# Kernel optimization log

Measured on AMD Instinct MI355X. Metric: run time of the kernel, lower is better.

## Reference

```python
import jax, jax.numpy as jnp
import numpy as np

N_HEAD = 16
N_EMBD = 1024


def setup_inputs() -> dict:
    key = jax.random.key(0)
    k1, k2, k3 = jax.random.split(key, 3)
    B, T = 2, 2048
    x = jax.random.normal(k1, (B, T, N_EMBD), dtype=jnp.float32)
    w_attn = jax.random.normal(k2, (N_EMBD, 3 * N_EMBD), dtype=jnp.float32) * 0.02
    b_attn = jnp.zeros((3 * N_EMBD,), dtype=jnp.float32)
    w_proj = jax.random.normal(k3, (N_EMBD, N_EMBD), dtype=jnp.float32) * 0.02
    b_proj = jnp.zeros((N_EMBD,), dtype=jnp.float32)
    return {"x": x, "w_attn": w_attn, "b_attn": b_attn, "w_proj": w_proj, "b_proj": b_proj}


def _split_heads(t):
    # [B, T, E] -> [B, H, T, hd]
    B, T, E = t.shape
    return t.reshape(B, T, N_HEAD, E // N_HEAD).transpose(0, 2, 1, 3)


def reference(x, w_attn, b_attn, w_proj, b_proj):
    B, T, E = x.shape
    hd = E // N_HEAD
    c = x @ w_attn + b_attn                       # [B, T, 3E]
    q, k, v = jnp.split(c, 3, axis=2)
    q, k, v = _split_heads(q), _split_heads(k), _split_heads(v)  # [B,H,T,hd]
    present = jnp.stack((k, v), axis=1)           # [B, 2, H, T, hd]
    # scores, scaled by rsqrt(head_dim)
    w = jnp.einsum("bhqd,bhkd->bhqk", q, k) * jax.lax.rsqrt(jnp.float32(hd))
    # causal mask: w * mask + -1e9 * (1 - mask)  (faithful to the source)
    mask = jnp.tril(jnp.ones((T, T), dtype=w.dtype))[None, None]
    w = w * mask + (-1e9) * (1.0 - mask)
    w = jax.nn.softmax(w, axis=-1)
    a = jnp.einsum("bhqk,bhkd->bhqd", w, v)       # [B,H,T,hd]
    a = a.transpose(0, 2, 1, 3).reshape(B, T, E)  # merge heads
    a = a @ w_proj + b_proj
    return a, present
```

## Files before the change

kernel.cpp:

```cpp
#include <hip/hip_runtime.h>

typedef unsigned short u16b;
typedef __attribute__((ext_vector_type(4))) float f32x4;
typedef __attribute__((ext_vector_type(8))) short bf16x8;

#define GLD_LDS(g, l) __builtin_amdgcn_global_load_lds( \
    (__attribute__((address_space(1))) void*)(g), \
    (__attribute__((address_space(3))) void*)(l), 16, 0, 0)

__device__ __forceinline__ u16b f2bf(float f) {
    unsigned u = __builtin_bit_cast(unsigned, f);
    u += 0x7fffu + ((u >> 16) & 1u);
    return (u16b)(u >> 16);
}
__device__ __forceinline__ unsigned trunc_bf(float f) {
    return __builtin_bit_cast(unsigned, f) >> 16;
}

__global__ void prep(const float* __restrict__ x, u16b* __restrict__ xb,
                     const float* __restrict__ w_attn, u16b* __restrict__ wab,
                     const float* __restrict__ w_proj, u16b* __restrict__ wpb) {
    __shared__ float tile[32][33];
    const int blk = blockIdx.x;
    if (blk < 4096) {
        int i = blk * 256 + threadIdx.x;
        float4 v = ((const float4*)x)[i];
        uint2 o;
        o.x = (unsigned)f2bf(v.x) | ((unsigned)f2bf(v.y) << 16);
        o.y = (unsigned)f2bf(v.z) | ((unsigned)f2bf(v.w) << 16);
        ((uint2*)xb)[i] = o;
        return;
    }
    const float* in;
    u16b* out;
    int idx, N;
    if (blk < 7168) { idx = blk - 4096; N = 3072; in = w_attn; out = wab; }
    else            { idx = blk - 7168; N = 1024; in = w_proj; out = wpb; }
    const int K = 1024;
    int kt = (idx & 31) * 32, nt = (idx >> 5) * 32;
    int c = threadIdx.x & 31, r8 = threadIdx.x >> 5;
    for (int i = 0; i < 4; i++) {
        int r = r8 + i * 8;
        tile[r][c] = in[(size_t)(kt + r) * N + nt + c];
    }
    __syncthreads();
    for (int i = 0; i < 4; i++) {
        int r = r8 + i * 8;
        out[(size_t)(nt + r) * K + kt + c] = f2bf(tile[c][r]);
    }
}

__global__ void trans_v(const u16b* __restrict__ in, u16b* __restrict__ out) {
    __shared__ u16b tile[64][66];
    const int bh = blockIdx.y;
    const int t0 = blockIdx.x * 64;
    const u16b* ip = in + (size_t)bh * 2048 * 64 + (size_t)t0 * 64;
    u16b* op = out + (size_t)bh * 64 * 2048 + t0;
    const int c = threadIdx.x & 7, r = threadIdx.x >> 3;
    #pragma unroll
    for (int it = 0; it < 2; it++) {
        int row = it * 32 + r;
        uint4 v = *(const uint4*)(ip + row * 64 + c * 8);
        const u16b* pv = (const u16b*)&v;
        #pragma unroll
        for (int e = 0; e < 8; e++) tile[c * 8 + e][row] = pv[e];
    }
    __syncthreads();
    const int d = threadIdx.x >> 2, c2 = threadIdx.x & 3;
    uint4 o[2];
    u16b* po = (u16b*)o;
    #pragma unroll
    for (int k = 0; k < 16; k++) po[k] = tile[d][c2 * 16 + k];
    *(uint4*)(op + d * 2048 + c2 * 16) = o[0];
    *(uint4*)(op + d * 2048 + c2 * 16 + 8) = o[1];
}

template<int EPI, int MI, int NI>
__global__ __launch_bounds__(256, 2) void gemm_bt(
    const u16b* __restrict__ A, const u16b* __restrict__ Bt,
    int M, int N, int K,
    const float* __restrict__ bias,
    float* __restrict__ out_f,
    u16b* __restrict__ q_ws, u16b* __restrict__ k_ws, u16b* __restrict__ v_ws)
{
    __shared__ u16b sA[(MI * 32) * 64];
    __shared__ u16b sB[(NI * 32) * 64];
    const int tid = threadIdx.x;
    const int l = tid & 63, w = tid >> 6;
    const int lr = l & 15, lg = l >> 4;
    const int m0 = blockIdx.y * (MI * 32), n0 = blockIdx.x * (NI * 32);
    const int wm = (w >> 1) * (MI * 16), wn = (w & 1) * (NI * 16);
    f32x4 acc[MI][NI] = {};

    for (int kt = 0; kt < K; kt += 64) {
        #pragma unroll
        for (int i = 0; i < MI; i++) {
            int chunk = i * 256 + tid;
            int row = chunk >> 3;
            int cb = (chunk & 7) ^ (row & 7);
            GLD_LDS(A + (size_t)(m0 + row) * K + kt + cb * 8, &sA[(i * 256 + w * 64) * 8]);
        }
        #pragma unroll
        for (int i = 0; i < NI; i++) {
            int chunk = i * 256 + tid;
            int row = chunk >> 3;
            int cb = (chunk & 7) ^ (row & 7);
            GLD_LDS(Bt + (size_t)(n0 + row) * K + kt + cb * 8, &sB[(i * 256 + w * 64) * 8]);
        }
        __syncthreads();
        #pragma unroll
        for (int ks = 0; ks < 2; ks++) {
            bf16x8 af[MI], bf[NI];
            #pragma unroll
            for (int i = 0; i < MI; i++) {
                int arow = wm + i * 16 + lr;
                af[i] = *(const bf16x8*)((const char*)sA + arow * 128 + ((ks * 64 + lg * 16) ^ ((arow & 7) << 4)));
            }
            #pragma unroll
            for (int i = 0; i < NI; i++) {
                int brow = wn + i * 16 + lr;
                bf[i] = *(const bf16x8*)((const char*)sB + brow * 128 + ((ks * 64 + lg * 16) ^ ((brow & 7) << 4)));
            }
            #pragma unroll
            for (int mi = 0; mi < MI; mi++)
                #pragma unroll
                for (int ni = 0; ni < NI; ni++)
                    acc[mi][ni] = __builtin_amdgcn_mfma_f32_16x16x32_bf16(af[mi], bf[ni], acc[mi][ni], 0, 0, 0);
        }
        __syncthreads();
    }

    if (EPI == 1) {
        #pragma unroll
        for (int ni = 0; ni < NI; ni++) {
            int col = n0 + wn + ni * 16 + lr;
            float bv = bias[col];
            #pragma unroll
            for (int mi = 0; mi < MI; mi++)
                #pragma unroll
                for (int jj = 0; jj < 4; jj++) {
                    int rowm = m0 + wm + mi * 16 + lg * 4 + jj;
                    out_f[(size_t)rowm * N + col] = acc[mi][ni][jj] + bv;
                }
        }
    } else {
        const int qkv = n0 >> 10;
        #pragma unroll
        for (int ni = 0; ni < NI; ni++) {
            int n = n0 + wn + ni * 16 + lr;
            float bv = bias[n];
            int h = (n >> 6) & 15, d = n & 63;
            #pragma unroll
            for (int mi = 0; mi < MI; mi++)
                #pragma unroll
                for (int jj = 0; jj < 4; jj++) {
                    int m = m0 + wm + mi * 16 + lg * 4 + jj;
                    int b = m >> 11, t = m & 2047;
                    float c = acc[mi][ni][jj] + bv;
                    size_t bhtd = ((size_t)(b * 16 + h) * 2048 + t) * 64 + d;
                    if (qkv == 0) {
                        q_ws[bhtd] = f2bf(c * 0.18033688011f);
                    } else if (qkv == 1) {
                        out_f[((size_t)((b * 2 + 0) * 16 + h) * 2048 + t) * 64 + d] = c;
                        k_ws[bhtd] = f2bf(c);
                    } else {
                        out_f[((size_t)((b * 2 + 1) * 16 + h) * 2048 + t) * 64 + d] = c;
                        v_ws[bhtd] = f2bf(c);
                    }
                }
        }
    }
}

__global__ __launch_bounds__(256, 4) void attn_fwd(
    const u16b* __restrict__ q_ws, const u16b* __restrict__ k_ws,
    const u16b* __restrict__ v_t, u16b* __restrict__ a_ws)
{
    __shared__ u16b sK[2][64 * 64];
    __shared__ u16b sV[2][64 * 64];
    __shared__ u16b sP[4][16 * 64];
    const int tid = threadIdx.x;
    const int l = tid & 63, w = tid >> 6;
    const int lr = l & 15, lg = l >> 4;
    const int g = blockIdx.x >> 5, bh = blockIdx.x & 31;
    const int a = g & 7, bq = g >> 3;
    const int qt = (bq == 0) ? a : (bq == 1) ? 15 - a : (bq == 2) ? 16 + a : 31 - a;
    const int b = bh >> 4, h = bh & 15;
    const size_t kbase = (size_t)bh * 2048 * 64;
    const size_t vbase = (size_t)bh * 64 * 2048;

    const int chunk0 = tid, chunk1 = 256 + tid;
    const int row0 = chunk0 >> 3, cb0 = (chunk0 & 7) ^ (row0 & 7);
    const int row1 = chunk1 >> 3, cb1 = (chunk1 & 7) ^ (row1 & 7);
    const u16b* kp0 = k_ws + kbase + (size_t)row0 * 64 + cb0 * 8;
    const u16b* kp1 = k_ws + kbase + (size_t)row1 * 64 + cb1 * 8;
    const u16b* vp0 = v_t + vbase + (size_t)row0 * 2048 + cb0 * 8;
    const u16b* vp1 = v_t + vbase + (size_t)row1 * 2048 + cb1 * 8;

    bf16x8 qf[2];
    {
        const u16b* qp = q_ws + kbase + (size_t)(qt * 64 + w * 16 + lr) * 64 + lg * 8;
        qf[0] = *(const bf16x8*)qp;
        qf[1] = *(const bf16x8*)(qp + 32);
    }
    const bf16x8 ones = {0x3F80, 0x3F80, 0x3F80, 0x3F80, 0x3F80, 0x3F80, 0x3F80, 0x3F80};
    f32x4 Oacc[4] = {};
    f32x4 Lacc = {};

    GLD_LDS(kp0, &sK[0][chunk0 * 8]);
    GLD_LDS(kp1, &sK[0][chunk1 * 8]);
    GLD_LDS(vp0, &sV[0][chunk0 * 8]);
    GLD_LDS(vp1, &sV[0][chunk1 * 8]);
    __syncthreads();
    int cur = 0;

    #pragma unroll 1
    for (int j = 0; j <= qt; j++) {
        if (j < qt) {
            int nxt = cur ^ 1;
            size_t ko = (size_t)(j + 1) * 64 * 64;
            size_t vo = (size_t)(j + 1) * 64;
            GLD_LDS(kp0 + ko, &sK[nxt][chunk0 * 8]);
            GLD_LDS(kp1 + ko, &sK[nxt][chunk1 * 8]);
            GLD_LDS(vp0 + vo, &sV[nxt][chunk0 * 8]);
            GLD_LDS(vp1 + vo, &sV[nxt][chunk1 * 8]);
        }
        const u16b* cK = &sK[cur][0];
        const u16b* cV = &sV[cur][0];

        f32x4 S[4];
        __builtin_amdgcn_s_setprio(1);
        #pragma unroll
        for (int c = 0; c < 4; c++) {
            f32x4 s = {};
            #pragma unroll
            for (int ks = 0; ks < 2; ks++) {
                int krow = c * 16 + lr;
                bf16x8 kf = *(const bf16x8*)((const char*)cK + krow * 128 + ((ks * 64 + lg * 16) ^ ((krow & 7) << 4)));
                s = __builtin_amdgcn_mfma_f32_16x16x32_bf16(kf, qf[ks], s, 0, 0, 0);
            }
            S[c] = s;
        }
        __builtin_amdgcn_s_setprio(0);
        if (j == qt) {
            const int ql = w * 16 + lr;
            #pragma unroll
            for (int c = 0; c < 4; c++)
                #pragma unroll
                for (int jj = 0; jj < 4; jj++)
                    if (c * 16 + lg * 4 + jj > ql) S[c][jj] = -1e9f;
        }
        u16b* myP = &sP[w][0];
        #pragma unroll
        for (int c = 0; c < 4; c++) {
            #pragma unroll
            for (int jj = 0; jj < 4; jj++)
                S[c][jj] = __builtin_amdgcn_exp2f(S[c][jj]);
            uint2 pk;
            pk.x = trunc_bf(S[c][0]) | (trunc_bf(S[c][1]) << 16);
            pk.y = trunc_bf(S[c][2]) | (trunc_bf(S[c][3]) << 16);
            *(uint2*)((char*)myP + lr * 128 + ((c * 32 + lg * 8) ^ ((lr & 7) << 4))) = pk;
        }
        __builtin_amdgcn_s_setprio(1);
        #pragma unroll
        for (int ks = 0; ks < 2; ks++) {
            bf16x8 pa = *(const bf16x8*)((const char*)myP + lr * 128 + ((ks * 64 + lg * 16) ^ ((lr & 7) << 4)));
            #pragma unroll
            for (int dc = 0; dc < 4; dc++) {
                int vrow = dc * 16 + lr;
                bf16x8 vb = *(const bf16x8*)((const char*)cV + vrow * 128 + ((ks * 64 + lg * 16) ^ ((vrow & 7) << 4)));
                Oacc[dc] = __builtin_amdgcn_mfma_f32_16x16x32_bf16(pa, vb, Oacc[dc], 0, 0, 0);
            }
            Lacc = __builtin_amdgcn_mfma_f32_16x16x32_bf16(pa, ones, Lacc, 0, 0, 0);
        }
        __builtin_amdgcn_s_setprio(0);
        __syncthreads();
        cur ^= 1;
    }
    #pragma unroll
    for (int jj = 0; jj < 4; jj++) {
        float inv = 1.f / Lacc[jj];
        int q = qt * 64 + w * 16 + lg * 4 + jj;
        #pragma unroll
        for (int dc = 0; dc < 4; dc++) {
            int d = dc * 16 + lr;
            a_ws[(size_t)(b * 2048 + q) * 1024 + h * 64 + d] = f2bf(Oacc[dc][jj] * inv);
        }
    }
}

extern "C" void kernel_launch(void* const* d_in, const int* in_sizes, int n_in,
                              void* d_out, int out_size, void* d_ws, size_t ws_size,
                              hipStream_t stream) {
    const float* x      = (const float*)d_in[0];
    const float* w_attn = (const float*)d_in[1];
    const float* b_attn = (const float*)d_in[2];
    const float* w_proj = (const float*)d_in[3];
    const float* b_proj = (const float*)d_in[4];
    float* out = (float*)d_out;
    float* present = out + 4194304;

    char* ws = (char*)d_ws;
    u16b* xb   = (u16b*)(ws);
    u16b* wab  = (u16b*)(ws + 8388608);
    u16b* wpb  = (u16b*)(ws + 14680064);
    u16b* q_ws = (u16b*)(ws + 16777216);
    u16b* k_ws = (u16b*)(ws + 25165824);
    u16b* v_ws = (u16b*)(ws + 33554432);
    u16b* a_ws = (u16b*)(ws + 41943040);
    u16b* v_t  = xb;

    prep<<<8192, 256, 0, stream>>>(x, xb, w_attn, wab, w_proj, wpb);
    gemm_bt<0, 2, 4><<<dim3(24, 64), 256, 0, stream>>>(xb, wab, 4096, 3072, 1024, b_attn,
                                                       present, q_ws, k_ws, v_ws);
    trans_v<<<dim3(32, 32), 256, 0, stream>>>(v_ws, v_t);
    attn_fwd<<<1024, 256, 0, stream>>>(q_ws, k_ws, v_t, a_ws);
    gemm_bt<1, 2, 2><<<dim3(16, 64), 256, 0, stream>>>(a_ws, wpb, 4096, 1024, 1024, b_proj,
                                                       out, nullptr, nullptr, nullptr);
}
```

Baseline: 115.5 us.

## Widen attention query tile to 128 rows with 8 waves sharing K/V loads

The attention kernel now uses 512-thread blocks with 8 waves covering 128 query rows, so each K/V tile loaded into LDS is reused by twice as many queries and the number of blocks is halved. Causal masking is applied over the last two KV tiles, and load balancing pairs query tiles g and 23-g. The QKV GEMM also switches to a larger M tile configuration with half the grid rows. The cost is fewer, heavier blocks, which may reduce occupancy and makes the causal diagonal waste more work per block.

```diff
diff --git a/kernel.cpp b/kernel.cpp
--- a/kernel.cpp
+++ b/kernel.cpp
@@ -172,58 +172,48 @@
     }
 }
 
-__global__ __launch_bounds__(256, 4) void attn_fwd(
+__global__ __launch_bounds__(512, 2) void attn_fwd(
     const u16b* __restrict__ q_ws, const u16b* __restrict__ k_ws,
     const u16b* __restrict__ v_t, u16b* __restrict__ a_ws)
 {
     __shared__ u16b sK[2][64 * 64];
     __shared__ u16b sV[2][64 * 64];
-    __shared__ u16b sP[4][16 * 64];
+    __shared__ u16b sP[8][16 * 64];
     const int tid = threadIdx.x;
     const int l = tid & 63, w = tid >> 6;
     const int lr = l & 15, lg = l >> 4;
     const int g = blockIdx.x >> 5, bh = blockIdx.x & 31;
-    const int a = g & 7, bq = g >> 3;
-    const int qt = (bq == 0) ? a : (bq == 1) ? 15 - a : (bq == 2) ? 16 + a : 31 - a;
+    const int qt = (g < 8) ? g : 23 - g;
     const int b = bh >> 4, h = bh & 15;
     const size_t kbase = (size_t)bh * 2048 * 64;
     const size_t vbase = (size_t)bh * 64 * 2048;
 
-    const int chunk0 = tid, chunk1 = 256 + tid;
-    const int row0 = chunk0 >> 3, cb0 = (chunk0 & 7) ^ (row0 & 7);
-    const int row1 = chunk1 >> 3, cb1 = (chunk1 & 7) ^ (row1 & 7);
+    const int row0 = tid >> 3, cb0 = (tid & 7) ^ (row0 & 7);
     const u16b* kp0 = k_ws + kbase + (size_t)row0 * 64 + cb0 * 8;
-    const u16b* kp1 = k_ws + kbase + (size_t)row1 * 64 + cb1 * 8;
     const u16b* vp0 = v_t + vbase + (size_t)row0 * 2048 + cb0 * 8;
-    const u16b* vp1 = v_t + vbase + (size_t)row1 * 2048 + cb1 * 8;
 
     bf16x8 qf[2];
     {
-        const u16b* qp = q_ws + kbase + (size_t)(qt * 64 + w * 16 + lr) * 64 + lg * 8;
+        const u16b* qp = q_ws + kbase + (size_t)(qt * 128 + w * 16 + lr) * 64 + lg * 8;
         qf[0] = *(const bf16x8*)qp;
         qf[1] = *(const bf16x8*)(qp + 32);
     }
     const bf16x8 ones = {0x3F80, 0x3F80, 0x3F80, 0x3F80, 0x3F80, 0x3F80, 0x3F80, 0x3F80};
     f32x4 Oacc[4] = {};
     f32x4 Lacc = {};
-
-    GLD_LDS(kp0, &sK[0][chunk0 * 8]);
-    GLD_LDS(kp1, &sK[0][chunk1 * 8]);
-    GLD_LDS(vp0, &sV[0][chunk0 * 8]);
-    GLD_LDS(vp1, &sV[0][chunk1 * 8]);
+    const int nj = 2 * qt + 2;
+
+    GLD_LDS(kp0, &sK[0][tid * 8]);
+    GLD_LDS(vp0, &sV[0][tid * 8]);
     __syncthreads();
     int cur = 0;
 
     #pragma unroll 1
-    for (int j = 0; j <= qt; j++) {
-        if (j < qt) {
+    for (int j = 0; j < nj; j++) {
+        if (j + 1 < nj) {
             int nxt = cur ^ 1;
-            size_t ko = (size_t)(j + 1) * 64 * 64;
-            size_t vo = (size_t)(j + 1) * 64;
-            GLD_LDS(kp0 + ko, &sK[nxt][chunk0 * 8]);
-            GLD_LDS(kp1 + ko, &sK[nxt][chunk1 * 8]);
-            GLD_LDS(vp0 + vo, &sV[nxt][chunk0 * 8]);
-            GLD_LDS(vp1 + vo, &sV[nxt][chunk1 * 8]);
+            GLD_LDS(kp0 + (size_t)(j + 1) * 64 * 64, &sK[nxt][tid * 8]);
+            GLD_LDS(vp0 + (size_t)(j + 1) * 64, &sV[nxt][tid * 8]);
         }
         const u16b* cK = &sK[cur][0];
         const u16b* cV = &sV[cur][0];
@@ -242,13 +232,14 @@
             S[c] = s;
         }
         __builtin_amdgcn_s_setprio(0);
-        if (j == qt) {
-            const int ql = w * 16 + lr;
+        if (j >= 2 * qt) {
+            const int qgl = qt * 128 + w * 16 + lr;
+            const int kv0 = j * 64;
             #pragma unroll
             for (int c = 0; c < 4; c++)
                 #pragma unroll
                 for (int jj = 0; jj < 4; jj++)
-                    if (c * 16 + lg * 4 + jj > ql) S[c][jj] = -1e9f;
+                    if (kv0 + c * 16 + lg * 4 + jj > qgl) S[c][jj] = -1e9f;
         }
         u16b* myP = &sP[w][0];
         #pragma unroll
@@ -280,7 +271,7 @@
     #pragma unroll
     for (int jj = 0; jj < 4; jj++) {
         float inv = 1.f / Lacc[jj];
-        int q = qt * 64 + w * 16 + lg * 4 + jj;
+        int q = qt * 128 + w * 16 + lg * 4 + jj;
         #pragma unroll
         for (int dc = 0; dc < 4; dc++) {
             int d = dc * 16 + lr;
@@ -311,10 +302,10 @@
     u16b* v_t  = xb;
 
     prep<<<8192, 256, 0, stream>>>(x, xb, w_attn, wab, w_proj, wpb);
-    gemm_bt<0, 2, 4><<<dim3(24, 64), 256, 0, stream>>>(xb, wab, 4096, 3072, 1024, b_attn,
+    gemm_bt<0, 4, 4><<<dim3(24, 32), 256, 0, stream>>>(xb, wab, 4096, 3072, 1024, b_attn,
                                                        present, q_ws, k_ws, v_ws);
     trans_v<<<dim3(32, 32), 256, 0, stream>>>(v_ws, v_t);
-    attn_fwd<<<1024, 256, 0, stream>>>(q_ws, k_ws, v_t, a_ws);
+    attn_fwd<<<512, 512, 0, stream>>>(q_ws, k_ws, v_t, a_ws);
     gemm_bt<1, 2, 2><<<dim3(16, 64), 256, 0, stream>>>(a_ws, wpb, 4096, 1024, 1024, b_proj,
                                                        out, nullptr, nullptr, nullptr);
 }
```

Result: faster. 112.8 us (-2.3%).

## Replace QKV GEMM with triple-buffered 128x128 tile kernel using async LDS loads

Applied to the files above, without the earlier changes.

Adds a dedicated QKV projection kernel with 128x128 output tiles, K-step 32 and a three-stage LDS ring filled by direct global-to-LDS loads. Each stage waits only on the oldest outstanding loads, and reads use an XOR swizzle to avoid bank conflicts. MFMA sections are wrapped in raised wave priority. The goal is to overlap global loads with MFMA work and raise data reuse per block, at the cost of higher register pressure from 16 accumulators per wave and a grid of only 768 blocks.

```diff
diff --git a/kernel.cpp b/kernel.cpp
--- a/kernel.cpp
+++ b/kernel.cpp
@@ -73,6 +73,116 @@
     for (int k = 0; k < 16; k++) po[k] = tile[d][c2 * 16 + k];
     *(uint4*)(op + d * 2048 + c2 * 16) = o[0];
     *(uint4*)(op + d * 2048 + c2 * 16 + 8) = o[1];
+}
+
+__global__ __launch_bounds__(256, 2) void gemm_ring_qkv(
+    const u16b* __restrict__ A, const u16b* __restrict__ Bt,
+    int M, int N, int K,
+    const float* __restrict__ bias,
+    float* __restrict__ out_f,
+    u16b* __restrict__ q_ws, u16b* __restrict__ k_ws, u16b* __restrict__ v_ws)
+{
+    __shared__ u16b sA[3][128 * 32];
+    __shared__ u16b sB[3][128 * 32];
+    const int tid = threadIdx.x;
+    const int l = tid & 63, w = tid >> 6;
+    const int lr = l & 15, lg = l >> 4;
+    const int m0 = blockIdx.y * 128, n0 = blockIdx.x * 128;
+    const int wm = (w >> 1) * 64, wn = (w & 1) * 64;
+    f32x4 acc[4][4] = {};
+
+    int srow[2], scb[2];
+    #pragma unroll
+    for (int i = 0; i < 2; i++) {
+        int chunk = i * 256 + tid;
+        srow[i] = chunk >> 2;
+        scb[i] = (chunk & 3) ^ (srow[i] & 3);
+    }
+
+#define STAGE_T(t)                                                                \
+    {                                                                             \
+        const int _b = (t) % 3;                                                   \
+        const int _kt = (t) * 32;                                                 \
+        _Pragma("unroll")                                                         \
+        for (int i = 0; i < 2; i++) {                                             \
+            int chunk = i * 256 + tid;                                            \
+            GLD_LDS(A + (size_t)(m0 + srow[i]) * K + _kt + scb[i] * 8,            \
+                    &sA[_b][chunk * 8]);                                          \
+            GLD_LDS(Bt + (size_t)(n0 + srow[i]) * K + _kt + scb[i] * 8,           \
+                    &sB[_b][chunk * 8]);                                          \
+        }                                                                         \
+    }
+
+    const int sw = (lg ^ (lr & 3)) << 4;
+
+#define COMPUTE_T(t)                                                              \
+    {                                                                             \
+        const int _b = (t) % 3;                                                   \
+        const char* bAp = (const char*)&sA[_b][0];                                \
+        const char* bBp = (const char*)&sB[_b][0];                                \
+        bf16x8 af[4], bf[4];                                                      \
+        _Pragma("unroll")                                                         \
+        for (int i = 0; i < 4; i++) {                                             \
+            int ar = wm + i * 16 + lr;                                            \
+            af[i] = *(const bf16x8*)(bAp + ar * 64 + sw);                         \
+            int br = wn + i * 16 + lr;                                            \
+            bf[i] = *(const bf16x8*)(bBp + br * 64 + sw);                         \
+        }                                                                         \
+        __builtin_amdgcn_s_setprio(1);                                            \
+        _Pragma("unroll")                                                         \
+        for (int mi = 0; mi < 4; mi++)                                            \
+            _Pragma("unroll")                                                     \
+            for (int ni = 0; ni < 4; ni++)                                        \
+                acc[mi][ni] = __builtin_amdgcn_mfma_f32_16x16x32_bf16(            \
+                    af[mi], bf[ni], acc[mi][ni], 0, 0, 0);                        \
+        __builtin_amdgcn_s_setprio(0);                                            \
+    }
+
+    const int NT = K >> 5;
+    STAGE_T(0);
+    STAGE_T(1);
+    asm volatile("s_waitcnt vmcnt(4)" ::: "memory");
+    __builtin_amdgcn_s_barrier();
+
+    #pragma unroll 1
+    for (int t = 0; t < NT - 2; ++t) {
+        STAGE_T(t + 2);
+        COMPUTE_T(t);
+        asm volatile("s_waitcnt vmcnt(4)" ::: "memory");
+        __builtin_amdgcn_s_barrier();
+    }
+    COMPUTE_T(NT - 2);
+    asm volatile("s_waitcnt vmcnt(0)" ::: "memory");
+    __builtin_amdgcn_s_barrier();
+    COMPUTE_T(NT - 1);
+#undef STAGE_T
+#undef COMPUTE_T
+
+    const int qkv = n0 >> 10;
+    #pragma unroll
+    for (int ni = 0; ni < 4; ni++) {
+        int n = n0 + wn + ni * 16 + lr;
+        float bv = bias[n];
+        int h = (n >> 6) & 15, d = n & 63;
+        #pragma unroll
+        for (int mi = 0; mi < 4; mi++)
+            #pragma unroll
+            for (int jj = 0; jj < 4; jj++) {
+                int m = m0 + wm + mi * 16 + lg * 4 + jj;
+                int b = m >> 11, t = m & 2047;
+                float c = acc[mi][ni][jj] + bv;
+                size_t bhtd = ((size_t)(b * 16 + h) * 2048 + t) * 64 + d;
+                if (qkv == 0) {
+                    q_ws[bhtd] = f2bf(c * 0.18033688011f);
+                } else if (qkv == 1) {
+                    out_f[((size_t)((b * 2 + 0) * 16 + h) * 2048 + t) * 64 + d] = c;
+                    k_ws[bhtd] = f2bf(c);
+                } else {
+                    out_f[((size_t)((b * 2 + 1) * 16 + h) * 2048 + t) * 64 + d] = c;
+                    v_ws[bhtd] = f2bf(c);
+                }
+            }
+    }
 }
 
 template<int EPI, int MI, int NI>
@@ -143,32 +253,6 @@
                     out_f[(size_t)rowm * N + col] = acc[mi][ni][jj] + bv;
                 }
         }
-    } else {
-        const int qkv = n0 >> 10;
-        #pragma unroll
-        for (int ni = 0; ni < NI; ni++) {
-            int n = n0 + wn + ni * 16 + lr;
-            float bv = bias[n];
-            int h = (n >> 6) & 15, d = n & 63;
-            #pragma unroll
-            for (int mi = 0; mi < MI; mi++)
-                #pragma unroll
-                for (int jj = 0; jj < 4; jj++) {
-                    int m = m0 + wm + mi * 16 + lg * 4 + jj;
-                    int b = m >> 11, t = m & 2047;
-                    float c = acc[mi][ni][jj] + bv;
-                    size_t bhtd = ((size_t)(b * 16 + h) * 2048 + t) * 64 + d;
-                    if (qkv == 0) {
-                        q_ws[bhtd] = f2bf(c * 0.18033688011f);
-                    } else if (qkv == 1) {
-                        out_f[((size_t)((b * 2 + 0) * 16 + h) * 2048 + t) * 64 + d] = c;
-                        k_ws[bhtd] = f2bf(c);
-                    } else {
-                        out_f[((size_t)((b * 2 + 1) * 16 + h) * 2048 + t) * 64 + d] = c;
-                        v_ws[bhtd] = f2bf(c);
-                    }
-                }
-        }
     }
 }
 
@@ -311,8 +395,8 @@
     u16b* v_t  = xb;
 
     prep<<<8192, 256, 0, stream>>>(x, xb, w_attn, wab, w_proj, wpb);
-    gemm_bt<0, 2, 4><<<dim3(24, 64), 256, 0, stream>>>(xb, wab, 4096, 3072, 1024, b_attn,
-                                                       present, q_ws, k_ws, v_ws);
+    gemm_ring_qkv<<<dim3(24, 32), 256, 0, stream>>>(xb, wab, 4096, 3072, 1024, b_attn,
+                                                    present, q_ws, k_ws, v_ws);
     trans_v<<<dim3(32, 32), 256, 0, stream>>>(v_ws, v_t);
     attn_fwd<<<1024, 256, 0, stream>>>(q_ws, k_ws, v_t, a_ws);
     gemm_bt<1, 2, 2><<<dim3(16, 64), 256, 0, stream>>>(a_ws, wpb, 4096, 1024, 1024, b_proj,
```

Measured after the change: 116.2 us. No clear change (+0.6%).

## Fuse V transpose into QKV GEMM epilogue and enlarge its M tile

Applied to the files above, without the earlier changes.

The QKV GEMM epilogue now writes V directly in transposed [b,h,d,t] layout, packing four consecutive time steps into one 8-byte store. This removes the separate trans_v kernel launch and its extra read and write of V. The QKV GEMM tile also grows from MI=2 to MI=4, which halves the grid and raises reuse of each B tile. The larger tile increases register and LDS use per block and may lower occupancy, and the transposed V stores are strided by 2048 elements across lanes.

```diff
diff --git a/kernel.cpp b/kernel.cpp
--- a/kernel.cpp
+++ b/kernel.cpp
@@ -50,38 +50,13 @@
     }
 }
 
-__global__ void trans_v(const u16b* __restrict__ in, u16b* __restrict__ out) {
-    __shared__ u16b tile[64][66];
-    const int bh = blockIdx.y;
-    const int t0 = blockIdx.x * 64;
-    const u16b* ip = in + (size_t)bh * 2048 * 64 + (size_t)t0 * 64;
-    u16b* op = out + (size_t)bh * 64 * 2048 + t0;
-    const int c = threadIdx.x & 7, r = threadIdx.x >> 3;
-    #pragma unroll
-    for (int it = 0; it < 2; it++) {
-        int row = it * 32 + r;
-        uint4 v = *(const uint4*)(ip + row * 64 + c * 8);
-        const u16b* pv = (const u16b*)&v;
-        #pragma unroll
-        for (int e = 0; e < 8; e++) tile[c * 8 + e][row] = pv[e];
-    }
-    __syncthreads();
-    const int d = threadIdx.x >> 2, c2 = threadIdx.x & 3;
-    uint4 o[2];
-    u16b* po = (u16b*)o;
-    #pragma unroll
-    for (int k = 0; k < 16; k++) po[k] = tile[d][c2 * 16 + k];
-    *(uint4*)(op + d * 2048 + c2 * 16) = o[0];
-    *(uint4*)(op + d * 2048 + c2 * 16 + 8) = o[1];
-}
-
 template<int EPI, int MI, int NI>
 __global__ __launch_bounds__(256, 2) void gemm_bt(
     const u16b* __restrict__ A, const u16b* __restrict__ Bt,
     int M, int N, int K,
     const float* __restrict__ bias,
     float* __restrict__ out_f,
-    u16b* __restrict__ q_ws, u16b* __restrict__ k_ws, u16b* __restrict__ v_ws)
+    u16b* __restrict__ q_ws, u16b* __restrict__ k_ws, u16b* __restrict__ v_t)
 {
     __shared__ u16b sA[(MI * 32) * 64];
     __shared__ u16b sB[(NI * 32) * 64];
@@ -151,23 +126,34 @@
             float bv = bias[n];
             int h = (n >> 6) & 15, d = n & 63;
             #pragma unroll
-            for (int mi = 0; mi < MI; mi++)
+            for (int mi = 0; mi < MI; mi++) {
+                const int mbase = m0 + wm + mi * 16 + lg * 4;
+                const int b = mbase >> 11, tb = mbase & 2047;
+                float cv[4];
                 #pragma unroll
-                for (int jj = 0; jj < 4; jj++) {
-                    int m = m0 + wm + mi * 16 + lg * 4 + jj;
-                    int b = m >> 11, t = m & 2047;
-                    float c = acc[mi][ni][jj] + bv;
-                    size_t bhtd = ((size_t)(b * 16 + h) * 2048 + t) * 64 + d;
-                    if (qkv == 0) {
-                        q_ws[bhtd] = f2bf(c * 0.18033688011f);
-                    } else if (qkv == 1) {
-                        out_f[((size_t)((b * 2 + 0) * 16 + h) * 2048 + t) * 64 + d] = c;
-                        k_ws[bhtd] = f2bf(c);
-                    } else {
-                        out_f[((size_t)((b * 2 + 1) * 16 + h) * 2048 + t) * 64 + d] = c;
-                        v_ws[bhtd] = f2bf(c);
+                for (int jj = 0; jj < 4; jj++)
+                    cv[jj] = acc[mi][ni][jj] + bv;
+                if (qkv == 0) {
+                    #pragma unroll
+                    for (int jj = 0; jj < 4; jj++)
+                        q_ws[((size_t)(b * 16 + h) * 2048 + tb + jj) * 64 + d] =
+                            f2bf(cv[jj] * 0.18033688011f);
+                } else if (qkv == 1) {
+                    #pragma unroll
+                    for (int jj = 0; jj < 4; jj++) {
+                        out_f[((size_t)((b * 2 + 0) * 16 + h) * 2048 + tb + jj) * 64 + d] = cv[jj];
+                        k_ws[((size_t)(b * 16 + h) * 2048 + tb + jj) * 64 + d] = f2bf(cv[jj]);
                     }
+                } else {
+                    #pragma unroll
+                    for (int jj = 0; jj < 4; jj++)
+                        out_f[((size_t)((b * 2 + 1) * 16 + h) * 2048 + tb + jj) * 64 + d] = cv[jj];
+                    uint2 pk;
+                    pk.x = (unsigned)f2bf(cv[0]) | ((unsigned)f2bf(cv[1]) << 16);
+                    pk.y = (unsigned)f2bf(cv[2]) | ((unsigned)f2bf(cv[3]) << 16);
+                    *(uint2*)(v_t + ((size_t)((b * 16 + h) * 64 + d)) * 2048 + tb) = pk;
                 }
+            }
         }
     }
 }
@@ -306,14 +292,12 @@
     u16b* wpb  = (u16b*)(ws + 14680064);
     u16b* q_ws = (u16b*)(ws + 16777216);
     u16b* k_ws = (u16b*)(ws + 25165824);
-    u16b* v_ws = (u16b*)(ws + 33554432);
+    u16b* v_t  = (u16b*)(ws + 33554432);
     u16b* a_ws = (u16b*)(ws + 41943040);
-    u16b* v_t  = xb;
 
     prep<<<8192, 256, 0, stream>>>(x, xb, w_attn, wab, w_proj, wpb);
-    gemm_bt<0, 2, 4><<<dim3(24, 64), 256, 0, stream>>>(xb, wab, 4096, 3072, 1024, b_attn,
-                                                       present, q_ws, k_ws, v_ws);
-    trans_v<<<dim3(32, 32), 256, 0, stream>>>(v_ws, v_t);
+    gemm_bt<0, 4, 4><<<dim3(24, 32), 256, 0, stream>>>(xb, wab, 4096, 3072, 1024, b_attn,
+                                                       present, q_ws, k_ws, v_t);
     attn_fwd<<<1024, 256, 0, stream>>>(q_ws, k_ws, v_t, a_ws);
     gemm_bt<1, 2, 2><<<dim3(16, 64), 256, 0, stream>>>(a_ws, wpb, 4096, 1024, 1024, b_proj,
                                                        out, nullptr, nullptr, nullptr);
```

Result: faster. 100.5 us (median of 2 runs) (-13.0%).
